# Optimization experiments

Measured on AMD Instinct MI355X. Metric: run time of the kernel, lower is better.

The kernel has to match this reference:

```python
import jax, jax.numpy as jnp
import numpy as np

B, T, DIM, H = 2, 2048, 1024, 16
HD = DIM // H


def setup_inputs() -> dict:
    key = jax.random.key(0)
    k1, k2, k3 = jax.random.split(key, 3)
    std = 1.0 / np.sqrt(DIM)
    x = jax.random.normal(k1, (B, T, DIM), dtype=jnp.float32)
    # torch Linear(dim, 3*dim).weight is [3*dim, dim]; we store the transposed
    # [dim, 3*dim] layout so forward is x @ W_qkv (same math).
    W_qkv = jax.random.uniform(k2, (DIM, 3 * DIM), dtype=jnp.float32, minval=-std, maxval=std)
    W_proj = jax.random.uniform(k3, (DIM, DIM), dtype=jnp.float32, minval=-std, maxval=std)
    return {"x": x, "W_qkv": W_qkv, "W_proj": W_proj}


def reference(x, W_qkv, W_proj):
    Bv, Tv, C = x.shape
    # qkv projection -> [B, T, 3, H, HD] -> q,k,v each [B, H, T, HD]
    qkv = (x @ W_qkv).reshape(Bv, Tv, 3, H, HD)
    qkv = jnp.transpose(qkv, (2, 0, 3, 1, 4))
    q, k, v = qkv[0], qkv[1], qkv[2]
    scale = jnp.asarray(np.sqrt(HD), dtype=x.dtype)
    scores = jnp.einsum('bhqd,bhkd->bhqk', q, k) / scale
    causal = jnp.tril(jnp.ones((Tv, Tv), dtype=bool))  # [T, T]
    scores = jnp.where(causal[None, None, :, :], scores, -jnp.inf)
    attn = jax.nn.softmax(scores, axis=-1)  # [B, H, T, T]
    # entropy per query position, averaged over heads -> [B, T]
    entropy = -(attn * jnp.log(attn + 1e-9)).sum(axis=-1).mean(axis=1)
    # dropout is identity in eval mode
    out = jnp.einsum('bhqk,bhkd->bhqd', attn, v)
    out = jnp.transpose(out, (0, 2, 1, 3)).reshape(Bv, Tv, C)
    return out @ W_proj, entropy
```

## Files before the change

### kernel.cpp

```cpp
#include <hip/hip_runtime.h>


typedef unsigned short u16;
typedef __attribute__((ext_vector_type(8))) __bf16 bf16x8;
typedef __attribute__((ext_vector_type(4))) float float4v;

#define BQ 2
#define TQ 2048
#define DIMQ 1024
#define HQ 16
#define HDQ 64

__device__ __forceinline__ float4v mfma16(bf16x8 a, bf16x8 b, float4v c) {
    return __builtin_amdgcn_mfma_f32_16x16x32_bf16(a, b, c, 0, 0, 0);
}

__device__ __forceinline__ u16 f2bf(float f) {
    unsigned x = __float_as_uint(f);
    return (u16)((x + 0x7FFFu + ((x >> 16) & 1u)) >> 16);
}

__device__ __forceinline__ uint4 cvt8(float4 a, float4 b) {
    union { uint4 v; u16 u[8]; } r;
    r.u[0] = f2bf(a.x); r.u[1] = f2bf(a.y); r.u[2] = f2bf(a.z); r.u[3] = f2bf(a.w);
    r.u[4] = f2bf(b.x); r.u[5] = f2bf(b.y); r.u[6] = f2bf(b.z); r.u[7] = f2bf(b.w);
    return r.v;
}

__device__ __forceinline__ void async16(const u16* g, u16* l) {
    __builtin_amdgcn_global_load_lds(
        (const __attribute__((address_space(1))) void*)g,
        (__attribute__((address_space(3))) void*)l, 16, 0, 0);
}

__device__ __forceinline__ void plswap(unsigned& a, unsigned& b) {
    asm("v_permlane32_swap_b32 %0, %1" : "+v"(a), "+v"(b));
    asm("v_permlane16_swap_b32 %0, %1" : "+v"(a), "+v"(b));
}

__device__ __forceinline__ void tr_tile(
    const float* __restrict__ in, u16* __restrict__ out, int R, int C,
    int tx, int ty, int tid, float (*T)[68])
{
    const int k0 = ty * 64, n0 = tx * 64;
    {
        int r = tid >> 2, cc = (tid & 3) << 4;
        const float* src = in + (size_t)(k0 + r) * C + n0 + cc;
        float4 v0 = ((const float4*)src)[0];
        float4 v1 = ((const float4*)src)[1];
        float4 v2 = ((const float4*)src)[2];
        float4 v3 = ((const float4*)src)[3];
        *(float4*)&T[r][cc + 0]  = v0;
        *(float4*)&T[r][cc + 4]  = v1;
        *(float4*)&T[r][cc + 8]  = v2;
        *(float4*)&T[r][cc + 12] = v3;
    }
    __syncthreads();
    {
        int nr = tid >> 2, kc = (tid & 3) << 4;
        union { uint4 v; u16 u[8]; } o0, o1;
#pragma unroll
        for (int j = 0; j < 8; ++j) o0.u[j] = f2bf(T[kc + j][nr]);
#pragma unroll
        for (int j = 0; j < 8; ++j) o1.u[j] = f2bf(T[kc + 8 + j][nr]);
        u16* dst = out + (size_t)(n0 + nr) * R + k0 + kc;
        ((uint4*)dst)[0] = o0.v;
        *(uint4*)(dst + 8) = o1.v;
    }
}

__global__ __launch_bounds__(256) void prep_kernel(
    const float* __restrict__ x, const float* __restrict__ Wq,
    const float* __restrict__ Wp,
    u16* __restrict__ xb, u16* __restrict__ Wt, u16* __restrict__ Wpt)
{
    __shared__ float T[64][68];
    const int bx = blockIdx.x, tid = threadIdx.x;
    if (bx < 2048) {
        int i = (bx * 256 + tid) * 8;
        float4 a = *(const float4*)(x + i);
        float4 b = *(const float4*)(x + i + 4);
        *(uint4*)(xb + i) = cvt8(a, b);
    } else if (bx < 2816) {
        int bb = bx - 2048;
        tr_tile(Wq, Wt, DIMQ, 3 * DIMQ, bb % 48, bb / 48, tid, T);
    } else {
        int bb = bx - 2816;
        tr_tile(Wp, Wpt, DIMQ, DIMQ, bb & 15, bb >> 4, tid, T);
    }
}

__global__ __launch_bounds__(256) void tr_cvt(
    const float* __restrict__ in, u16* __restrict__ out, int R, int C)
{
    __shared__ float T[64][68];
    tr_tile(in, out, R, C, blockIdx.x, blockIdx.y, threadIdx.x, T);
}

template <int TILEM, int MODE>
__global__ __launch_bounds__(256) void gemm_db(
    const u16* __restrict__ A, const u16* __restrict__ Bt,
    int M, int N, int K,
    u16* __restrict__ Qo, u16* __restrict__ Ko, u16* __restrict__ Vt,
    float* __restrict__ Of, const float* __restrict__ EntIn)
{
    constexpr int MT = TILEM / 32;
    constexpr int AR = TILEM / 64;
    __shared__ u16 As[2][TILEM * 32];
    __shared__ u16 Bs[2][128 * 32];

    const int tid = threadIdx.x;
    const int nbn = gridDim.x;
    const int flat = blockIdx.y * nbn + blockIdx.x;
    const int cpx = (nbn * gridDim.y) >> 3;
    const int swz = (flat & 7) * cpx + (flat >> 3);
    const int bm = swz / nbn, bn = swz % nbn;
    const int wave = tid >> 6, lane = tid & 63;
    const int quad = lane >> 4, c = lane & 15;
    const int wm = wave >> 1, wn = wave & 1;
    const int x3 = c & 3;

    const float4v z = {0.f, 0.f, 0.f, 0.f};
    float4v acc[MT][4];
#pragma unroll
    for (int mt = 0; mt < MT; ++mt)
#pragma unroll
        for (int tn = 0; tn < 4; ++tn) acc[mt][tn] = z;

    const int srow = tid >> 2;
    const int schunk8 = (((tid & 3) ^ (srow & 3)) << 3);
    const u16* ga = A  + (size_t)(bm * TILEM + srow) * K + schunk8;
    const u16* gb = Bt + (size_t)(bn * 128  + srow) * K + schunk8;

#pragma unroll
    for (int p = 0; p < AR; ++p)
        async16(ga + (size_t)(p * 64) * K, As[0] + p * 2048 + tid * 8);
#pragma unroll
    for (int p = 0; p < 2; ++p)
        async16(gb + (size_t)(p * 64) * K, Bs[0] + p * 2048 + tid * 8);

    const int niter = K >> 5;
    for (int it = 0; it < niter; ++it) {
        __syncthreads();
        if (it + 1 < niter) {
            const int nb = (it + 1) & 1;
            const int kc = (it + 1) * 32;
#pragma unroll
            for (int p = 0; p < AR; ++p)
                async16(ga + kc + (size_t)(p * 64) * K, As[nb] + p * 2048 + tid * 8);
#pragma unroll
            for (int p = 0; p < 2; ++p)
                async16(gb + kc + (size_t)(p * 64) * K, Bs[nb] + p * 2048 + tid * 8);
        }
        const u16* as = As[it & 1];
        const u16* bs = Bs[it & 1];

        bf16x8 af[MT], bfr[4];
#pragma unroll
        for (int mt = 0; mt < MT; ++mt)
            af[mt] = *(const bf16x8*)&as[(wm * (TILEM / 2) + mt * 16 + c) * 32 +
                                         ((quad ^ x3) << 3)];
#pragma unroll
        for (int tn = 0; tn < 4; ++tn)
            bfr[tn] = *(const bf16x8*)&bs[(wn * 64 + tn * 16 + c) * 32 +
                                          ((quad ^ x3) << 3)];
#pragma unroll
        for (int mt = 0; mt < MT; ++mt)
#pragma unroll
            for (int tn = 0; tn < 4; ++tn)
                acc[mt][tn] = mfma16(af[mt], bfr[tn], acc[mt][tn]);
    }

#pragma unroll
    for (int mt = 0; mt < MT; ++mt)
#pragma unroll
        for (int tn = 0; tn < 4; ++tn) {
            int gm0 = bm * TILEM + wm * (TILEM / 2) + mt * 16 + quad * 4;
            int gn  = bn * 128 + wn * 64 + tn * 16 + c;
            if (MODE == 0) {
                int s = gn >> 10, h = (gn >> 6) & 15, d = gn & 63;
                int b = gm0 >> 11, t0 = gm0 & 2047;
                size_t bh = (size_t)(b * HQ + h);
                if (s == 2) {
                    union { unsigned long long w; u16 u[4]; } pk;
#pragma unroll
                    for (int r = 0; r < 4; ++r) pk.u[r] = f2bf(acc[mt][tn][r]);
                    *(unsigned long long*)&Vt[(bh * HDQ + d) * TQ + t0] = pk.w;
                } else {
                    u16* dst = (s == 0) ? Qo : Ko;
                    float sc = (s == 0) ? 0.18033688f : 1.0f;
#pragma unroll
                    for (int r = 0; r < 4; ++r)
                        dst[(bh * TQ + t0 + r) * HDQ + d] = f2bf(acc[mt][tn][r] * sc);
                }
            } else {
#pragma unroll
                for (int r = 0; r < 4; ++r)
                    Of[(size_t)(gm0 + r) * N + gn] = acc[mt][tn][r];
            }
        }

    if (MODE == 1 && bn == 0 && bm < 16) {
        int i = bm * 256 + tid;
        int b = i >> 11, t = i & 2047;
        float s = 0.f;
#pragma unroll
        for (int h = 0; h < HQ; ++h) s += EntIn[((size_t)(b * HQ + h)) * TQ + t];
        Of[(size_t)BQ * TQ * DIMQ + i] = s * (1.0f / HQ);
    }
}

__global__ __launch_bounds__(256) void attn_kernel(
    const u16* __restrict__ Q, const u16* __restrict__ K,
    const u16* __restrict__ Vt, u16* __restrict__ AO,
    float* __restrict__ Ent)
{
    const int d = blockIdx.x;
    const int j = d >> 3;
    const int bh = (d & 7) * 4 + (j >> 3);
    const int ptg = j & 7;
    const int qt[4] = { ptg, 8 + ptg, 23 - ptg, 31 - ptg };

    const int tid = threadIdx.x;
    const int wave = tid >> 6, lane = tid & 63;
    const int quad = lane >> 4, c = lane & 15;
    const int x7 = c & 7;

    __shared__ u16 Ks[2][64 * 64];
    __shared__ u16 Vs[2][64 * 64];

    const u16* Qp = Q  + (size_t)bh * TQ * HDQ;
    const u16* Kp = K  + (size_t)bh * TQ * HDQ;
    const u16* Vp = Vt + (size_t)bh * HDQ * TQ;

    int q0[4];
#pragma unroll
    for (int s = 0; s < 4; ++s) q0[s] = qt[s] * 64 + wave * 16;

    bf16x8 qf[4][2];
#pragma unroll
    for (int s = 0; s < 4; ++s) {
        const u16* qr = Qp + (size_t)(q0[s] + c) * HDQ;
        qf[s][0] = *(const bf16x8*)(qr + quad * 8);
        qf[s][1] = *(const bf16x8*)(qr + 32 + quad * 8);
    }

    const float MX2 = 17.312336f;
    const float4v z = {0.f, 0.f, 0.f, 0.f};
    const float4v mz = {-MX2, -MX2, -MX2, -MX2};
    float4v oacc[4][4];
#pragma unroll
    for (int s = 0; s < 4; ++s)
#pragma unroll
        for (int tn = 0; tn < 4; ++tn) oacc[s][tn] = z;
    float lp[4] = {0.f, 0.f, 0.f, 0.f}, tp[4] = {0.f, 0.f, 0.f, 0.f};

    const int ntile = qt[3] + 1;

    const int srow = tid >> 3;
    const int schunk8 = (((tid & 7) ^ (srow & 7)) << 3);
    const u16* ka = Kp + (size_t)srow * HDQ + schunk8;
    const u16* va = Vp + (size_t)srow * TQ + schunk8;

    {
        async16(ka, Ks[0] + tid * 8);
        async16(ka + (size_t)32 * HDQ, Ks[0] + 2048 + tid * 8);
        async16(va, Vs[0] + tid * 8);
        async16(va + (size_t)32 * TQ, Vs[0] + 2048 + tid * 8);
    }

    for (int jt = 0; jt < ntile; ++jt) {
        __syncthreads();
        if (jt + 1 < ntile) {
            int nb = (jt + 1) & 1;
            async16(ka + (size_t)((jt + 1) * 64) * HDQ, Ks[nb] + tid * 8);
            async16(ka + (size_t)((jt + 1) * 64 + 32) * HDQ, Ks[nb] + 2048 + tid * 8);
            async16(va + (jt + 1) * 64, Vs[nb] + tid * 8);
            async16(va + (size_t)32 * TQ + (jt + 1) * 64, Vs[nb] + 2048 + tid * 8);
        }
        const u16* ksb = Ks[jt & 1];
        const u16* vsb = Vs[jt & 1];

        bf16x8 kf[4][2], vf[4][2];
#pragma unroll
        for (int tn = 0; tn < 4; ++tn) {
            int base = (tn * 16 + c) * 64;
            kf[tn][0] = *(const bf16x8*)&ksb[base + ((quad ^ x7) << 3)];
            kf[tn][1] = *(const bf16x8*)&ksb[base + (((quad + 4) ^ x7) << 3)];
            vf[tn][0] = *(const bf16x8*)&vsb[base + ((quad ^ x7) << 3)];
            vf[tn][1] = *(const bf16x8*)&vsb[base + (((quad + 4) ^ x7) << 3)];
        }

#pragma unroll
        for (int s = 0; s < 4; ++s) {
            if (s < 3 && jt > qt[s]) continue;
            unsigned w0[4], w1[4];
#pragma unroll
            for (int tn = 0; tn < 4; ++tn) {
                float4v sacc = mz;
                sacc = mfma16(kf[tn][0], qf[s][0], sacc);
                sacc = mfma16(kf[tn][1], qf[s][1], sacc);
                if (jt == qt[s]) {
#pragma unroll
                    for (int r = 0; r < 4; ++r) {
                        int kg = jt * 64 + tn * 16 + quad * 4 + r;
                        if (kg > q0[s] + c) sacc[r] = -1e30f;
                    }
                }
                float pv[4];
#pragma unroll
                for (int r = 0; r < 4; ++r) {
                    float sv = sacc[r];
                    float p;
                    asm("v_exp_f32 %0, %1" : "=v"(p) : "v"(sv));
                    lp[s] += p;
                    tp[s] += p * sv;
                    pv[r] = p;
                }
                asm("v_cvt_pk_bf16_f32 %0, %1, %2"
                    : "=v"(w0[tn]) : "v"(pv[0]), "v"(pv[1]));
                asm("v_cvt_pk_bf16_f32 %0, %1, %2"
                    : "=v"(w1[tn]) : "v"(pv[2]), "v"(pv[3]));
            }
            plswap(w0[0], w0[1]);
            plswap(w1[0], w1[1]);
            plswap(w0[2], w0[3]);
            plswap(w1[2], w1[3]);
            union { uint4 u; bf16x8 v; } P0, P1;
            P0.u = (uint4){w0[0], w1[0], w0[1], w1[1]};
            P1.u = (uint4){w0[2], w1[2], w0[3], w1[3]};
            __builtin_amdgcn_s_setprio(1);
#pragma unroll
            for (int tn = 0; tn < 4; ++tn) {
                oacc[s][tn] = mfma16(vf[tn][0], P0.v, oacc[s][tn]);
                oacc[s][tn] = mfma16(vf[tn][1], P1.v, oacc[s][tn]);
            }
            __builtin_amdgcn_s_setprio(0);
        }
    }

    const int b = bh >> 4, h = bh & 15;
#pragma unroll
    for (int s = 0; s < 4; ++s) {
        float l = lp[s], t = tp[s];
        l += __shfl_xor(l, 16); l += __shfl_xor(l, 32);
        t += __shfl_xor(t, 16); t += __shfl_xor(t, 32);

        float inv = 1.0f / l;
        u16* dst = AO + ((size_t)(b * TQ + q0[s] + c)) * DIMQ + h * HDQ;
#pragma unroll
        for (int tn = 0; tn < 4; ++tn) {
            unsigned u[4];
#pragma unroll
            for (int r = 0; r < 4; ++r)
                u[r] = (unsigned)f2bf(oacc[s][tn][r] * inv);
            uint2 pk;
            pk.x = u[0] | (u[1] << 16);
            pk.y = u[2] | (u[3] << 16);
            *(uint2*)(dst + tn * 16 + quad * 4) = pk;
        }
        if (quad == 0)
            Ent[(size_t)bh * TQ + q0[s] + c] =
                __logf(l) - 0.69314718f * t / l;
    }
}

extern "C" void kernel_launch(void* const* d_in, const int* in_sizes, int n_in,
                              void* d_out, int out_size, void* d_ws, size_t ws_size,
                              hipStream_t stream) {
    const float* x     = (const float*)d_in[0];
    const float* Wqkv  = (const float*)d_in[1];
    const float* Wproj = (const float*)d_in[2];
    float* out = (float*)d_out;

    const size_t NE = (size_t)BQ * HQ * TQ * HDQ;
    const size_t WQN = (size_t)3 * DIMQ * DIMQ;
    const size_t WPN = (size_t)DIMQ * DIMQ;
    u16* Qb  = (u16*)d_ws;
    u16* Kb  = Qb + NE;
    u16* Vtb = Kb + NE;
    u16* xb  = Vtb + NE;
    u16* Wt  = xb + NE;
    u16* AO  = xb;

    const size_t need = (4 * NE + WQN + WPN) * 2 + (size_t)BQ * HQ * TQ * 4;
    const bool room = ws_size >= need;
    u16* Wpt = room ? (Wt + WQN) : Wt;
    float* Ent = room ? (float*)(Wpt + WPN) : (float*)(Wt + WQN);

    prep_kernel<<<dim3(room ? 3072 : 2816), 256, 0, stream>>>(
        x, Wqkv, Wproj, xb, Wt, Wpt);
    gemm_db<128, 0><<<dim3(24, 32), 256, 0, stream>>>(
        xb, Wt, BQ * TQ, 3 * DIMQ, DIMQ, Qb, Kb, Vtb, nullptr, nullptr);
    if (!room)
        tr_cvt<<<dim3(16, 16), 256, 0, stream>>>(Wproj, Wpt, DIMQ, DIMQ);
    attn_kernel<<<dim3(256), 256, 0, stream>>>(Qb, Kb, Vtb, AO, Ent);
    gemm_db<64, 1><<<dim3(8, 64), 256, 0, stream>>>(
        AO, Wpt, BQ * TQ, DIMQ, DIMQ, nullptr, nullptr, nullptr, out, Ent);
}
```

Baseline: 182.8 us.

## Split attention key tiles across wave pairs and double the grid

```diff
diff --git a/kernel.cpp b/kernel.cpp
--- a/kernel.cpp
+++ b/kernel.cpp
@@ -217,45 +217,52 @@
 {
     const int d = blockIdx.x;
     const int j = d >> 3;
-    const int bh = (d & 7) * 4 + (j >> 3);
-    const int ptg = j & 7;
-    const int qt[4] = { ptg, 8 + ptg, 23 - ptg, 31 - ptg };
+    const int bh = (d & 7) * 4 + (j >> 4);
+    int pt = j & 15;
+    if (j & 32) pt = 15 - pt;
+    const int qt[2] = { pt, 31 - pt };
 
     const int tid = threadIdx.x;
     const int wave = tid >> 6, lane = tid & 63;
+    const int kw = wave & 1;
+    const int qh = wave >> 1;
     const int quad = lane >> 4, c = lane & 15;
     const int x7 = c & 7;
 
     __shared__ u16 Ks[2][64 * 64];
     __shared__ u16 Vs[2][64 * 64];
+    __shared__ float Red[2][64][64];
+    __shared__ float lred[2][2][2][16], tred[2][2][2][16];
 
     const u16* Qp = Q  + (size_t)bh * TQ * HDQ;
     const u16* Kp = K  + (size_t)bh * TQ * HDQ;
     const u16* Vp = Vt + (size_t)bh * HDQ * TQ;
 
-    int q0[4];
-#pragma unroll
-    for (int s = 0; s < 4; ++s) q0[s] = qt[s] * 64 + wave * 16;
-
-    bf16x8 qf[4][2];
-#pragma unroll
-    for (int s = 0; s < 4; ++s) {
-        const u16* qr = Qp + (size_t)(q0[s] + c) * HDQ;
-        qf[s][0] = *(const bf16x8*)(qr + quad * 8);
-        qf[s][1] = *(const bf16x8*)(qr + 32 + quad * 8);
-    }
+    const int qb[2] = { qt[0] * 64 + qh * 32, qt[1] * 64 + qh * 32 };
+
+    bf16x8 qf[2][2][2];
+#pragma unroll
+    for (int s = 0; s < 2; ++s)
+#pragma unroll
+        for (int qs = 0; qs < 2; ++qs) {
+            const u16* qr = Qp + (size_t)(qb[s] + qs * 16 + c) * HDQ;
+            qf[s][qs][0] = *(const bf16x8*)(qr + quad * 8);
+            qf[s][qs][1] = *(const bf16x8*)(qr + 32 + quad * 8);
+        }
 
     const float MX2 = 17.312336f;
     const float4v z = {0.f, 0.f, 0.f, 0.f};
     const float4v mz = {-MX2, -MX2, -MX2, -MX2};
-    float4v oacc[4][4];
-#pragma unroll
-    for (int s = 0; s < 4; ++s)
-#pragma unroll
-        for (int tn = 0; tn < 4; ++tn) oacc[s][tn] = z;
-    float lp[4] = {0.f, 0.f, 0.f, 0.f}, tp[4] = {0.f, 0.f, 0.f, 0.f};
-
-    const int ntile = qt[3] + 1;
+    float4v oacc[2][2][4];
+#pragma unroll
+    for (int s = 0; s < 2; ++s)
+#pragma unroll
+        for (int qs = 0; qs < 2; ++qs)
+#pragma unroll
+            for (int tn = 0; tn < 4; ++tn) oacc[s][qs][tn] = z;
+    float lp[2][2] = {{0.f,0.f},{0.f,0.f}}, tp[2][2] = {{0.f,0.f},{0.f,0.f}};
+
+    const int ntile = qt[1] + 1;
 
     const int srow = tid >> 3;
     const int schunk8 = (((tid & 7) ^ (srow & 7)) << 3);
@@ -281,87 +288,126 @@
         const u16* ksb = Ks[jt & 1];
         const u16* vsb = Vs[jt & 1];
 
-        bf16x8 kf[4][2], vf[4][2];
-#pragma unroll
-        for (int tn = 0; tn < 4; ++tn) {
-            int base = (tn * 16 + c) * 64;
-            kf[tn][0] = *(const bf16x8*)&ksb[base + ((quad ^ x7) << 3)];
-            kf[tn][1] = *(const bf16x8*)&ksb[base + (((quad + 4) ^ x7) << 3)];
-            vf[tn][0] = *(const bf16x8*)&vsb[base + ((quad ^ x7) << 3)];
-            vf[tn][1] = *(const bf16x8*)&vsb[base + (((quad + 4) ^ x7) << 3)];
-        }
-
-#pragma unroll
-        for (int s = 0; s < 4; ++s) {
-            if (s < 3 && jt > qt[s]) continue;
-            unsigned w0[4], w1[4];
-#pragma unroll
-            for (int tn = 0; tn < 4; ++tn) {
-                float4v sacc = mz;
-                sacc = mfma16(kf[tn][0], qf[s][0], sacc);
-                sacc = mfma16(kf[tn][1], qf[s][1], sacc);
-                if (jt == qt[s]) {
+        bf16x8 kf[2][2], vf[4];
+#pragma unroll
+        for (int kt = 0; kt < 2; ++kt) {
+            int base = (kw * 32 + kt * 16 + c) * 64;
+            kf[kt][0] = *(const bf16x8*)&ksb[base + ((quad ^ x7) << 3)];
+            kf[kt][1] = *(const bf16x8*)&ksb[base + (((quad + 4) ^ x7) << 3)];
+        }
+#pragma unroll
+        for (int tn = 0; tn < 4; ++tn)
+            vf[tn] = *(const bf16x8*)&vsb[(tn * 16 + c) * 64 +
+                                          (((kw * 4 + quad) ^ x7) << 3)];
+
+#pragma unroll
+        for (int s = 0; s < 2; ++s) {
+            if (s == 0 && jt > qt[0]) continue;
+#pragma unroll
+            for (int qs = 0; qs < 2; ++qs) {
+                unsigned w0[2], w1[2];
+#pragma unroll
+                for (int kt = 0; kt < 2; ++kt) {
+                    float4v sacc = mz;
+                    sacc = mfma16(kf[kt][0], qf[s][qs][0], sacc);
+                    sacc = mfma16(kf[kt][1], qf[s][qs][1], sacc);
+                    if (jt == qt[s]) {
+#pragma unroll
+                        for (int r = 0; r < 4; ++r) {
+                            int kg = jt * 64 + kw * 32 + kt * 16 + quad * 4 + r;
+                            if (kg > qb[s] + qs * 16 + c) sacc[r] = -1e30f;
+                        }
+                    }
+                    float pv[4];
 #pragma unroll
                     for (int r = 0; r < 4; ++r) {
-                        int kg = jt * 64 + tn * 16 + quad * 4 + r;
-                        if (kg > q0[s] + c) sacc[r] = -1e30f;
+                        float sv = sacc[r];
+                        float p;
+                        asm("v_exp_f32 %0, %1" : "=v"(p) : "v"(sv));
+                        lp[s][qs] += p;
+                        tp[s][qs] += p * sv;
+                        pv[r] = p;
                     }
+                    asm("v_cvt_pk_bf16_f32 %0, %1, %2"
+                        : "=v"(w0[kt]) : "v"(pv[0]), "v"(pv[1]));
+                    asm("v_cvt_pk_bf16_f32 %0, %1, %2"
+                        : "=v"(w1[kt]) : "v"(pv[2]), "v"(pv[3]));
                 }
-                float pv[4];
-#pragma unroll
-                for (int r = 0; r < 4; ++r) {
-                    float sv = sacc[r];
-                    float p;
-                    asm("v_exp_f32 %0, %1" : "=v"(p) : "v"(sv));
-                    lp[s] += p;
-                    tp[s] += p * sv;
-                    pv[r] = p;
+                plswap(w0[0], w0[1]);
+                plswap(w1[0], w1[1]);
+                union { uint4 u; bf16x8 v; } P;
+                P.u = (uint4){w0[0], w1[0], w0[1], w1[1]};
+                __builtin_amdgcn_s_setprio(1);
+#pragma unroll
+                for (int tn = 0; tn < 4; ++tn)
+                    oacc[s][qs][tn] = mfma16(vf[tn], P.v, oacc[s][qs][tn]);
+                __builtin_amdgcn_s_setprio(0);
+            }
+        }
+    }
+
+    __syncthreads();
+#pragma unroll
+    for (int s = 0; s < 2; ++s)
+#pragma unroll
+        for (int qs = 0; qs < 2; ++qs) {
+            lp[s][qs] += __shfl_xor(lp[s][qs], 16);
+            lp[s][qs] += __shfl_xor(lp[s][qs], 32);
+            tp[s][qs] += __shfl_xor(tp[s][qs], 16);
+            tp[s][qs] += __shfl_xor(tp[s][qs], 32);
+        }
+
+    if (kw == 1) {
+#pragma unroll
+        for (int s = 0; s < 2; ++s)
+#pragma unroll
+            for (int qs = 0; qs < 2; ++qs) {
+#pragma unroll
+                for (int tn = 0; tn < 4; ++tn)
+#pragma unroll
+                    for (int r = 0; r < 4; ++r)
+                        Red[qh][((s * 2 + qs) * 4 + tn) * 4 + r][lane] =
+                            oacc[s][qs][tn][r];
+                if (quad == 0) {
+                    lred[qh][s][qs][c] = lp[s][qs];
+                    tred[qh][s][qs][c] = tp[s][qs];
                 }
-                asm("v_cvt_pk_bf16_f32 %0, %1, %2"
-                    : "=v"(w0[tn]) : "v"(pv[0]), "v"(pv[1]));
-                asm("v_cvt_pk_bf16_f32 %0, %1, %2"
-                    : "=v"(w1[tn]) : "v"(pv[2]), "v"(pv[3]));
             }
-            plswap(w0[0], w0[1]);
-            plswap(w1[0], w1[1]);
-            plswap(w0[2], w0[3]);
-            plswap(w1[2], w1[3]);
-            union { uint4 u; bf16x8 v; } P0, P1;
-            P0.u = (uint4){w0[0], w1[0], w0[1], w1[1]};
-            P1.u = (uint4){w0[2], w1[2], w0[3], w1[3]};
-            __builtin_amdgcn_s_setprio(1);
-#pragma unroll
-            for (int tn = 0; tn < 4; ++tn) {
-                oacc[s][tn] = mfma16(vf[tn][0], P0.v, oacc[s][tn]);
-                oacc[s][tn] = mfma16(vf[tn][1], P1.v, oacc[s][tn]);
+    }
+    __syncthreads();
+    if (kw == 0) {
+        const int b = bh >> 4, h = bh & 15;
+#pragma unroll
+        for (int s = 0; s < 2; ++s)
+#pragma unroll
+            for (int qs = 0; qs < 2; ++qs) {
+#pragma unroll
+                for (int tn = 0; tn < 4; ++tn)
+#pragma unroll
+                    for (int r = 0; r < 4; ++r)
+                        oacc[s][qs][tn][r] +=
+                            Red[qh][((s * 2 + qs) * 4 + tn) * 4 + r][lane];
+                float l = lp[s][qs] + lred[qh][s][qs][c];
+                float t = tp[s][qs] + tred[qh][s][qs][c];
+
+                float inv = 1.0f / l;
+                u16* dst = AO + ((size_t)(b * TQ + qb[s] + qs * 16 + c)) * DIMQ
+                           + h * HDQ;
+#pragma unroll
+                for (int tn = 0; tn < 4; ++tn) {
+                    unsigned u[4];
+#pragma unroll
+                    for (int r = 0; r < 4; ++r)
+                        u[r] = (unsigned)f2bf(oacc[s][qs][tn][r] * inv);
+                    uint2 pk;
+                    pk.x = u[0] | (u[1] << 16);
+                    pk.y = u[2] | (u[3] << 16);
+                    *(uint2*)(dst + tn * 16 + quad * 4) = pk;
+                }
+                if (quad == 0)
+                    Ent[(size_t)bh * TQ + qb[s] + qs * 16 + c] =
+                        __logf(l) - 0.69314718f * t / l;
             }
-            __builtin_amdgcn_s_setprio(0);
-        }
-    }
-
-    const int b = bh >> 4, h = bh & 15;
-#pragma unroll
-    for (int s = 0; s < 4; ++s) {
-        float l = lp[s], t = tp[s];
-        l += __shfl_xor(l, 16); l += __shfl_xor(l, 32);
-        t += __shfl_xor(t, 16); t += __shfl_xor(t, 32);
-
-        float inv = 1.0f / l;
-        u16* dst = AO + ((size_t)(b * TQ + q0[s] + c)) * DIMQ + h * HDQ;
-#pragma unroll
-        for (int tn = 0; tn < 4; ++tn) {
-            unsigned u[4];
-#pragma unroll
-            for (int r = 0; r < 4; ++r)
-                u[r] = (unsigned)f2bf(oacc[s][tn][r] * inv);
-            uint2 pk;
-            pk.x = u[0] | (u[1] << 16);
-            pk.y = u[2] | (u[3] << 16);
-            *(uint2*)(dst + tn * 16 + quad * 4) = pk;
-        }
-        if (quad == 0)
-            Ent[(size_t)bh * TQ + q0[s] + c] =
-                __logf(l) - 0.69314718f * t / l;
     }
 }
 
@@ -394,7 +440,7 @@
         xb, Wt, BQ * TQ, 3 * DIMQ, DIMQ, Qb, Kb, Vtb, nullptr, nullptr);
     if (!room)
         tr_cvt<<<dim3(16, 16), 256, 0, stream>>>(Wproj, Wpt, DIMQ, DIMQ);
-    attn_kernel<<<dim3(256), 256, 0, stream>>>(Qb, Kb, Vtb, AO, Ent);
+    attn_kernel<<<dim3(512), 256, 0, stream>>>(Qb, Kb, Vtb, AO, Ent);
     gemm_db<64, 1><<<dim3(8, 64), 256, 0, stream>>>(
         AO, Wpt, BQ * TQ, DIMQ, DIMQ, nullptr, nullptr, nullptr, out, Ent);
 }
```

Result: faster. 177.9 us (-2.7%).
